# Optimization experiments

Measured on AMD Instinct MI355X. Metric: run time of the kernel, lower is better.

The kernel has to match this reference:

```python
import jax, jax.numpy as jnp
import numpy as np

B, N, C = 2, 384, 1024          # images, proposals/image, box_head feature dim
H_REPN = 256                    # RePN hidden
G_HID, HEADS = 256, 4           # GATConv hidden / heads
TOPK = 8
IMG_H, IMG_W = 800, 800
NEG_SLOPE = 0.2                 # PyG GATConv leaky_relu default


def _box_geom(bx):
    # normalized [x, y, w, h], matching _box_geom
    scale = jnp.array([IMG_W, IMG_H, IMG_W, IMG_H], dtype=bx.dtype)
    nb = bx / scale
    return jnp.stack([nb[:, 0], nb[:, 1], nb[:, 2] - nb[:, 0], nb[:, 3] - nb[:, 1]], axis=1)


def _gat_layer(x, src, tgt, W, att_src, att_dst, bias, heads, out_c):
    # PyG GATConv: messages flow src -> tgt, softmax over incoming edges at tgt
    n = x.shape[0]
    xw = (x @ W).reshape(n, heads, out_c)               # [N, H, F]
    a_s = jnp.sum(xw * att_src, axis=-1)                # [N, H]
    a_d = jnp.sum(xw * att_dst, axis=-1)                # [N, H]
    e = jax.nn.leaky_relu(a_s[src] + a_d[tgt], NEG_SLOPE)  # [E, H]
    e_max = jax.ops.segment_max(e, tgt, num_segments=n)    # stable softmax per target
    alpha = jnp.exp(e - e_max[tgt])
    denom = jax.ops.segment_sum(alpha, tgt, num_segments=n)
    alpha = alpha / jnp.maximum(denom, 1e-16)[tgt]          # [E, H]
    out = jax.ops.segment_sum(xw[src] * alpha[..., None], tgt, num_segments=n)
    return out.reshape(n, heads * out_c) + bias


def setup_inputs() -> dict:
    key = jax.random.key(0)
    ks = jax.random.split(key, 16)
    feats = jax.random.normal(ks[0], (B, N, C), dtype=jnp.float32)
    # boxes with x1<x2, y1<y2 inside the image
    xy = jax.random.uniform(ks[1], (B, N, 2), minval=0.0, maxval=650.0)
    wh = jax.random.uniform(ks[2], (B, N, 2), minval=10.0, maxval=150.0)
    boxes = jnp.concatenate([xy, xy + wh], axis=-1).astype(jnp.float32)
    s = 0.02
    params = {
        'fc1_w': jax.random.normal(ks[3], (2 * C + 4, H_REPN)) * s,
        'fc1_b': jnp.zeros((H_REPN,), jnp.float32),
        'fc2_w': jax.random.normal(ks[4], (H_REPN, 1)) * s,
        'fc2_b': jnp.zeros((1,), jnp.float32),
        'gat1_w': jax.random.normal(ks[5], (C + 4, HEADS * G_HID)) * s,
        'gat1_att_src': jax.random.normal(ks[6], (HEADS, G_HID)) * s,
        'gat1_att_dst': jax.random.normal(ks[7], (HEADS, G_HID)) * s,
        'gat1_b': jnp.zeros((HEADS * G_HID,), jnp.float32),
        'gat2_w': jax.random.normal(ks[8], (HEADS * G_HID, 2)) * s,
        'gat2_att_src': jax.random.normal(ks[9], (1, 2)) * s,
        'gat2_att_dst': jax.random.normal(ks[10], (1, 2)) * s,
        'gat2_b': jnp.zeros((2,), jnp.float32),
    }
    return {'feats': feats, 'boxes': boxes, **params}


def reference(feats, boxes, fc1_w, fc1_b, fc2_w, fc2_b,
              gat1_w, gat1_att_src, gat1_att_dst, gat1_b,
              gat2_w, gat2_att_src, gat2_att_dst, gat2_b):
    def single(f, bx):
        geom4 = _box_geom(bx)                               # [N, 4]
        x = jnp.concatenate([f, geom4], axis=1)             # [N, C+4]
        # RelationProposalNetwork: fc1(cat[f_i, f_j, |b_i-b_j|]) done as split matmuls
        Wa, Wb, Wg = fc1_w[:C], fc1_w[C:2 * C], fc1_w[2 * C:]
        p1 = f @ Wa                                         # [N, H]
        p2 = f @ Wb                                         # [N, H]
        gdiff = jnp.abs(bx[:, None, :] - bx[None, :, :])    # [N, N, 4]
        h = jax.nn.relu(p1[:, None, :] + p2[None, :, :] + gdiff @ Wg + fc1_b)
        rel = (h @ fc2_w)[..., 0] + fc2_b[0]                # [N, N]
        # _make_edge_index: mask diagonal, top-k per row; edge = [dst_node, neighbor]
        rn = rel - jnp.eye(N, dtype=rel.dtype) * 1e6
        nbr = jax.lax.top_k(rn, TOPK)[1]                    # [N, k]
        src = jnp.repeat(jnp.arange(N), TOPK)               # edge_index[0] (PyG source)
        tgt = nbr.reshape(-1)                               # edge_index[1] (PyG target)
        loop = jnp.arange(N)                                # GATConv add_self_loops=True
        src = jnp.concatenate([src, loop])
        tgt = jnp.concatenate([tgt, loop])
        h1 = jax.nn.relu(_gat_layer(x, src, tgt, gat1_w, gat1_att_src, gat1_att_dst, gat1_b, HEADS, G_HID))
        logits = _gat_layer(h1, src, tgt, gat2_w, gat2_att_src, gat2_att_dst, gat2_b, 1, 2)
        return logits                                       # [N, 2]
    return jax.vmap(single)(feats, boxes)
```

## Files before the change

### kernel.cpp

```cpp
#include <hip/hip_runtime.h>

#define BB 2
#define NN 384
#define CC 1024
#define HR 256
#define NHEADS 4
#define TOPK 8
#define CAP 448
#define NEG 0.2f

typedef __attribute__((ext_vector_type(8))) short bf16x8;
typedef __attribute__((ext_vector_type(4))) float f32x4;

__device__ __forceinline__ unsigned short f2bf(float v) {
    unsigned u = __float_as_uint(v);
    return (unsigned short)((u + 0x7FFFu + ((u >> 16) & 1u)) >> 16);
}
__device__ __forceinline__ float bf2f(unsigned short h) {
    return __uint_as_float((unsigned)h << 16);
}

__global__ __launch_bounds__(256) void k_prep(const float* __restrict__ feats,
        const float* __restrict__ boxes, const float* __restrict__ gat1_w,
        const float* __restrict__ fc1_w,
        uint4* __restrict__ Asw, uint4* __restrict__ Bsw,
        uint4* __restrict__ Ah, uint4* __restrict__ Al,
        uint4* __restrict__ Bh, uint4* __restrict__ Bl,
        float4* __restrict__ wgp, int* __restrict__ counts,
        float* __restrict__ xw2) {
    int blk = blockIdx.x;
    int t = threadIdx.x;
    int gflat = blk * 256 + t;
    if (gflat < BB * NN) counts[gflat] = 0;
    if (gflat < BB * NN * 2) xw2[gflat] = 0.f;

    if (blk < 396) {
        int flat = gflat;
        int lane = flat & 63;
        int kc = (flat >> 6) % 33;
        int mt = flat / (33 * 64);
        int m = mt * 16 + (lane & 15);
        int k0 = kc * 32 + (lane >> 4) * 8;
        unsigned short vals[8];
        const float s = 1.0f / 800.0f;
#pragma unroll
        for (int j = 0; j < 8; j++) {
            int k = k0 + j;
            float v;
            if (k < CC) v = feats[(size_t)m * CC + k];
            else if (k < CC + 4) {
                const float* bx = boxes + (size_t)m * 4;
                int gk = k - CC;
                v = (gk == 0) ? bx[0] * s : (gk == 1) ? bx[1] * s
                  : (gk == 2) ? (bx[2] - bx[0]) * s : (bx[3] - bx[1]) * s;
            } else v = 0.f;
            vals[j] = f2bf(v);
        }
        uint4 pk;
        pk.x = (unsigned)vals[0] | ((unsigned)vals[1] << 16);
        pk.y = (unsigned)vals[2] | ((unsigned)vals[3] << 16);
        pk.z = (unsigned)vals[4] | ((unsigned)vals[5] << 16);
        pk.w = (unsigned)vals[6] | ((unsigned)vals[7] << 16);
        Asw[flat] = pk;
    } else if (blk < 924) {
        int flat = gflat - 396 * 256;
        int lane = flat & 63;
        int kc = (flat >> 6) % 33;
        int nt = flat / (33 * 64);
        int n = nt * 16 + (lane & 15);
        int k0 = kc * 32 + (lane >> 4) * 8;
        unsigned short vals[8];
#pragma unroll
        for (int j = 0; j < 8; j++) {
            int k = k0 + j;
            float v = (k < CC + 4) ? gat1_w[(size_t)k * 1024 + n] : 0.f;
            vals[j] = f2bf(v);
        }
        uint4 pk;
        pk.x = (unsigned)vals[0] | ((unsigned)vals[1] << 16);
        pk.y = (unsigned)vals[2] | ((unsigned)vals[3] << 16);
        pk.z = (unsigned)vals[4] | ((unsigned)vals[5] << 16);
        pk.w = (unsigned)vals[6] | ((unsigned)vals[7] << 16);
        Bsw[flat] = pk;
    } else if (blk < 1308) {
        int flat = gflat - 924 * 256;
        int lane = flat & 63;
        int kc = (flat >> 6) % 32;
        int mt = flat / (32 * 64);
        int m = mt * 16 + (lane & 15);
        int k0 = kc * 32 + (lane >> 4) * 8;
        unsigned short vh[8], vl[8];
        const float* src = feats + (size_t)m * CC + k0;
#pragma unroll
        for (int j = 0; j < 8; j++) {
            float v = src[j];
            unsigned short h = f2bf(v);
            vh[j] = h;
            vl[j] = f2bf(v - bf2f(h));
        }
        uint4 ph, pl;
        ph.x = (unsigned)vh[0] | ((unsigned)vh[1] << 16);
        ph.y = (unsigned)vh[2] | ((unsigned)vh[3] << 16);
        ph.z = (unsigned)vh[4] | ((unsigned)vh[5] << 16);
        ph.w = (unsigned)vh[6] | ((unsigned)vh[7] << 16);
        pl.x = (unsigned)vl[0] | ((unsigned)vl[1] << 16);
        pl.y = (unsigned)vl[2] | ((unsigned)vl[3] << 16);
        pl.z = (unsigned)vl[4] | ((unsigned)vl[5] << 16);
        pl.w = (unsigned)vl[6] | ((unsigned)vl[7] << 16);
        Ah[flat] = ph; Al[flat] = pl;
    } else if (blk < 1564) {
        int flat = gflat - 1308 * 256;
        int lane = flat & 63;
        int kc = (flat >> 6) % 32;
        int nt = flat / (32 * 64);
        int n = nt * 16 + (lane & 15);
        int k0 = kc * 32 + (lane >> 4) * 8;
        unsigned short vh[8], vl[8];
#pragma unroll
        for (int j = 0; j < 8; j++) {
            int k = k0 + j;
            float v = (n < 256) ? fc1_w[(size_t)k * 256 + n]
                                : fc1_w[(size_t)(CC + k) * 256 + (n - 256)];
            unsigned short h = f2bf(v);
            vh[j] = h;
            vl[j] = f2bf(v - bf2f(h));
        }
        uint4 ph, pl;
        ph.x = (unsigned)vh[0] | ((unsigned)vh[1] << 16);
        ph.y = (unsigned)vh[2] | ((unsigned)vh[3] << 16);
        ph.z = (unsigned)vh[4] | ((unsigned)vh[5] << 16);
        ph.w = (unsigned)vh[6] | ((unsigned)vh[7] << 16);
        pl.x = (unsigned)vl[0] | ((unsigned)vl[1] << 16);
        pl.y = (unsigned)vl[2] | ((unsigned)vl[3] << 16);
        pl.z = (unsigned)vl[4] | ((unsigned)vl[5] << 16);
        pl.w = (unsigned)vl[6] | ((unsigned)vl[7] << 16);
        Bh[flat] = ph; Bl[flat] = pl;
    } else {
        int c = t;
        float4 w;
        w.x = fc1_w[(size_t)(2 * CC + 0) * HR + c];
        w.y = fc1_w[(size_t)(2 * CC + 1) * HR + c];
        w.z = fc1_w[(size_t)(2 * CC + 2) * HR + c];
        w.w = fc1_w[(size_t)(2 * CC + 3) * HR + c];
        wgp[c] = w;
    }
}

__global__ __launch_bounds__(512) void k_mm(const uint4* __restrict__ Ah,
        const uint4* __restrict__ Al, const uint4* __restrict__ Bh,
        const uint4* __restrict__ Bl, const float* __restrict__ fc1_b,
        float* __restrict__ p1, float* __restrict__ p2t,
        const uint4* __restrict__ Asw, const uint4* __restrict__ Bsw,
        float* __restrict__ xw1) {
    __shared__ float lds[4][64][4];
    int t = threadIdx.x;
    int w = t >> 6;
    int lane = t & 63;
    int g = w & 3;
    int kh = w >> 2;
    int blk0 = blockIdx.x;
    if (blk0 < 384) {
        int blk = blk0;
        int mt = blk >> 3;
        int nt = (blk & 7) * 4 + g;
        f32x4 acc = {0.f, 0.f, 0.f, 0.f};
        const uint4* pah = Ah + (size_t)mt * 32 * 64 + (size_t)kh * 16 * 64 + lane;
        const uint4* pal = Al + (size_t)mt * 32 * 64 + (size_t)kh * 16 * 64 + lane;
        const uint4* pbh = Bh + (size_t)nt * 32 * 64 + (size_t)kh * 16 * 64 + lane;
        const uint4* pbl = Bl + (size_t)nt * 32 * 64 + (size_t)kh * 16 * 64 + lane;
#pragma unroll 4
        for (int kc = 0; kc < 16; kc++) {
            uint4 ah = pah[kc * 64];
            uint4 al = pal[kc * 64];
            uint4 bh = pbh[kc * 64];
            uint4 bl = pbl[kc * 64];
            acc = __builtin_amdgcn_mfma_f32_16x16x32_bf16(*(bf16x8*)&ah, *(bf16x8*)&bh, acc, 0, 0, 0);
            acc = __builtin_amdgcn_mfma_f32_16x16x32_bf16(*(bf16x8*)&ah, *(bf16x8*)&bl, acc, 0, 0, 0);
            acc = __builtin_amdgcn_mfma_f32_16x16x32_bf16(*(bf16x8*)&al, *(bf16x8*)&bh, acc, 0, 0, 0);
        }
        if (kh == 1) {
#pragma unroll
            for (int r = 0; r < 4; r++) lds[g][lane][r] = acc[r];
        }
        __syncthreads();
        if (kh == 0) {
#pragma unroll
            for (int r = 0; r < 4; r++) acc[r] += lds[g][lane][r];
            int col = nt * 16 + (lane & 15);
            int row0 = mt * 16 + (lane >> 4) * 4;
            if (col < 256) {
                float bias = fc1_b[col];
#pragma unroll
                for (int r = 0; r < 4; r++)
                    p1[(size_t)(row0 + r) * 256 + col] = acc[r] + bias;
            } else {
#pragma unroll
                for (int r = 0; r < 4; r++) {
                    int rr = row0 + r;
                    int b = rr / NN, rloc = rr % NN;
                    p2t[((size_t)b * 256 + (col - 256)) * NN + rloc] = acc[r];
                }
            }
        }
    } else {
        int blk = blk0 - 384;
        int mt = blk >> 4;
        int nt = (blk & 15) * 4 + g;
        int nk = kh ? 16 : 17;
        f32x4 acc = {0.f, 0.f, 0.f, 0.f};
        const uint4* pa = Asw + (size_t)mt * 33 * 64 + (size_t)kh * 17 * 64 + lane;
        const uint4* pb = Bsw + (size_t)nt * 33 * 64 + (size_t)kh * 17 * 64 + lane;
#pragma unroll 4
        for (int kc = 0; kc < nk; kc++) {
            uint4 av = pa[kc * 64];
            uint4 bv = pb[kc * 64];
            acc = __builtin_amdgcn_mfma_f32_16x16x32_bf16(*(bf16x8*)&av, *(bf16x8*)&bv, acc, 0, 0, 0);
        }
        if (kh == 1) {
#pragma unroll
            for (int r = 0; r < 4; r++) lds[g][lane][r] = acc[r];
        }
        __syncthreads();
        if (kh == 0) {
#pragma unroll
            for (int r = 0; r < 4; r++) acc[r] += lds[g][lane][r];
            int col = nt * 16 + (lane & 15);
            int row0 = mt * 16 + (lane >> 4) * 4;
#pragma unroll
            for (int r = 0; r < 4; r++)
                xw1[(size_t)(row0 + r) * 1024 + col] = acc[r];
        }
    }
}

__global__ __launch_bounds__(384) void k_relatt(const float* __restrict__ p1,
        const float* __restrict__ p2t, const float* __restrict__ boxes,
        const float4* __restrict__ wgp, const float* __restrict__ fc2_w,
        float* __restrict__ rel_a, float* __restrict__ rel_b,
        const float* __restrict__ xw1, const float* __restrict__ att_src,
        const float* __restrict__ att_dst, float* __restrict__ a_s,
        float* __restrict__ a_d) {
    int blk0 = blockIdx.x;
    if (blk0 < 768) {
        int blk = blk0;
        int p = blk >> 1;
        int ch = blk & 1;
        int b = p / (NN / 2);
        int i0 = (p - b * (NN / 2)) * 2;
        int row0 = b * NN + i0;
        int j = threadIdx.x;
        float a0 = boxes[(size_t)row0 * 4 + 0];
        float a1 = boxes[(size_t)row0 * 4 + 1];
        float a2 = boxes[(size_t)row0 * 4 + 2];
        float a3 = boxes[(size_t)row0 * 4 + 3];
        float c0 = boxes[(size_t)(row0 + 1) * 4 + 0];
        float c1 = boxes[(size_t)(row0 + 1) * 4 + 1];
        float c2 = boxes[(size_t)(row0 + 1) * 4 + 2];
        float c3 = boxes[(size_t)(row0 + 1) * 4 + 3];
        float4 bj = *(const float4*)(boxes + ((size_t)b * NN + j) * 4);
        float g00 = fabsf(a0 - bj.x), g01 = fabsf(a1 - bj.y);
        float g02 = fabsf(a2 - bj.z), g03 = fabsf(a3 - bj.w);
        float g10 = fabsf(c0 - bj.x), g11 = fabsf(c1 - bj.y);
        float g12 = fabsf(c2 - bj.z), g13 = fabsf(c3 - bj.w);
        const float* p1r0 = p1 + (size_t)row0 * HR + ch * 128;
        const float* p1r1 = p1r0 + HR;
        const float* p2b = p2t + (size_t)b * HR * NN + (size_t)ch * 128 * NN + j;
        const float4* wg = wgp + ch * 128;
        const float* w2 = fc2_w + ch * 128;
        float acc0 = 0.f, acc1 = 0.f;
#pragma unroll 8
        for (int c = 0; c < 128; c++) {
            float4 w = wg[c];
            float pa = p1r0[c];
            float pb = p1r1[c];
            float wc = w2[c];
            float p2v = p2b[(size_t)c * NN];
            float v0 = pa + p2v + g00 * w.x + g01 * w.y + g02 * w.z + g03 * w.w;
            float v1 = pb + p2v + g10 * w.x + g11 * w.y + g12 * w.z + g13 * w.w;
            acc0 += fmaxf(v0, 0.f) * wc;
            acc1 += fmaxf(v1, 0.f) * wc;
        }
        float* dst = ch ? rel_b : rel_a;
        dst[(size_t)row0 * NN + j] = acc0;
        dst[(size_t)(row0 + 1) * NN + j] = acc1;
    } else {
        int node = blk0 - 768;
        int t = threadIdx.x;
        if (t >= 256) return;
        int w = t >> 6;
        int lane = t & 63;
        const float4* xr = (const float4*)(xw1 + (size_t)node * 1024 + w * 256);
        const float4* sr = (const float4*)(att_src + w * 256);
        const float4* dr = (const float4*)(att_dst + w * 256);
        float4 x = xr[lane];
        float4 s = sr[lane];
        float4 d = dr[lane];
        float ps = x.x * s.x + x.y * s.y + x.z * s.z + x.w * s.w;
        float pd = x.x * d.x + x.y * d.y + x.z * d.z + x.w * d.w;
#pragma unroll
        for (int off = 32; off > 0; off >>= 1) {
            ps += __shfl_xor(ps, off);
            pd += __shfl_xor(pd, off);
        }
        if (lane == 0) {
            a_s[(size_t)node * NHEADS + w] = ps;
            a_d[(size_t)node * NHEADS + w] = pd;
        }
    }
}

__global__ __launch_bounds__(64) void k_topk_inv(const float* __restrict__ rel_a,
        const float* __restrict__ rel_b, int* __restrict__ counts,
        int* __restrict__ inlist) {
    int row = blockIdx.x;
    int b = row / NN;
    int i = row - b * NN;
    int t = threadIdx.x;
    const float* ra = rel_a + (size_t)row * NN;
    const float* rb = rel_b + (size_t)row * NN;
    float v[6]; int id[6];
#pragma unroll
    for (int q = 0; q < 6; q++) {
        int j = t + q * 64;
        float val = ra[j] + rb[j];
        if (j == i) val = -INFINITY;
        v[q] = val; id[q] = j;
    }
    int mine = -1;
    for (int k = 0; k < TOPK; k++) {
        float bv = -INFINITY; int bi = NN;
#pragma unroll
        for (int q = 0; q < 6; q++) {
            if (v[q] > bv || (v[q] == bv && id[q] < bi)) { bv = v[q]; bi = id[q]; }
        }
        for (int off = 32; off > 0; off >>= 1) {
            float ov = __shfl_down(bv, off);
            int   oi = __shfl_down(bi, off);
            if (ov > bv || (ov == bv && oi < bi)) { bv = ov; bi = oi; }
        }
        bi = __shfl(bi, 0);
        if (t == k) mine = bi;
#pragma unroll
        for (int q = 0; q < 6; q++) if (id[q] == bi) v[q] = -INFINITY;
    }
    if (t < TOPK) {
        int tg = b * NN + mine;
        int q = atomicAdd(&counts[tg], 1);
        inlist[(size_t)tg * CAP + q] = i;
    } else if (t == TOPK) {
        int q = atomicAdd(&counts[row], 1);
        inlist[(size_t)row * CAP + q] = i;
    }
}

__global__ __launch_bounds__(256) void k_agg1h(const int* __restrict__ counts,
        const int* __restrict__ inlist, const float* __restrict__ a_s,
        const float* __restrict__ a_d, const float* __restrict__ xw1,
        const float* __restrict__ gat1_b, const float* __restrict__ w2,
        float* __restrict__ xw2) {
    __shared__ int slist[CAP];
    __shared__ float walpha[CAP];
    __shared__ float redp[8];
    int blk = blockIdx.x;
    int node = blk >> 2;
    int h = blk & 3;
    int b = node / NN;
    int t = threadIdx.x;
    int wid = t >> 6;
    int lane = t & 63;
    int deg = counts[node];
    for (int e = t; e < deg; e += 256) slist[e] = inlist[(size_t)node * CAP + e];
    __syncthreads();
    if (t < 64) {
        float ad = a_d[(size_t)node * NHEADS + h];
        float vals[7];
        int cnt = 0;
        float vmax = -INFINITY;
        for (int e = t; e < deg; e += 64) {
            float x = a_s[(size_t)(b * NN + slist[e]) * NHEADS + h] + ad;
            x = x >= 0.f ? x : NEG * x;
            vals[cnt++] = x;
            vmax = fmaxf(vmax, x);
        }
#pragma unroll
        for (int off = 32; off > 0; off >>= 1)
            vmax = fmaxf(vmax, __shfl_xor(vmax, off));
        float sum = 0.f;
        for (int i = 0; i < cnt; i++) {
            vals[i] = expf(vals[i] - vmax);
            sum += vals[i];
        }
#pragma unroll
        for (int off = 32; off > 0; off >>= 1)
            sum += __shfl_xor(sum, off);
        float inv = 1.f / fmaxf(sum, 1e-16f);
        cnt = 0;
        for (int e = t; e < deg; e += 64) walpha[e] = vals[cnt++] * inv;
    }
    __syncthreads();
    float acc = 0.f;
    for (int e = 0; e < deg; e++)
        acc += walpha[e] * xw1[(size_t)(b * NN + slist[e]) * 1024 + h * 256 + t];
    float o = fmaxf(acc + gat1_b[h * 256 + t], 0.f);
    int d = h * 256 + t;
    float p0 = o * w2[d * 2];
    float p1v = o * w2[d * 2 + 1];
#pragma unroll
    for (int off = 32; off > 0; off >>= 1) {
        p0 += __shfl_xor(p0, off);
        p1v += __shfl_xor(p1v, off);
    }
    if (lane == 0) { redp[wid] = p0; redp[4 + wid] = p1v; }
    __syncthreads();
    if (t == 0) {
        atomicAdd(&xw2[(size_t)node * 2],     redp[0] + redp[1] + redp[2] + redp[3]);
        atomicAdd(&xw2[(size_t)node * 2 + 1], redp[4] + redp[5] + redp[6] + redp[7]);
    }
}

__global__ __launch_bounds__(64) void k_agg2(const int* __restrict__ counts,
        const int* __restrict__ inlist, const float* __restrict__ xw2,
        const float* __restrict__ as2, const float* __restrict__ ad2,
        const float* __restrict__ b2, float* __restrict__ out) {
    int node = blockIdx.x;
    int b = node / NN;
    int lane = threadIdx.x;
    int deg = counts[node];
    float s0 = as2[0], s1 = as2[1];
    float d0 = ad2[0], d1 = ad2[1];
    float2 xwn = *(const float2*)(xw2 + (size_t)node * 2);
    float ad = xwn.x * d0 + xwn.y * d1;
    float vals[7], xs0[7], xs1[7];
    int cnt = 0;
    float vmax = -INFINITY;
    for (int e = lane; e < deg; e += 64) {
        int s = b * NN + inlist[(size_t)node * CAP + e];
        float2 xws = *(const float2*)(xw2 + (size_t)s * 2);
        float x = xws.x * s0 + xws.y * s1 + ad;
        x = x >= 0.f ? x : NEG * x;
        xs0[cnt] = xws.x; xs1[cnt] = xws.y; vals[cnt] = x; cnt++;
        vmax = fmaxf(vmax, x);
    }
#pragma unroll
    for (int off = 32; off > 0; off >>= 1)
        vmax = fmaxf(vmax, __shfl_xor(vmax, off));
    float sum = 0.f;
    for (int i = 0; i < cnt; i++) {
        vals[i] = expf(vals[i] - vmax);
        sum += vals[i];
    }
#pragma unroll
    for (int off = 32; off > 0; off >>= 1)
        sum += __shfl_xor(sum, off);
    float inv = 1.f / fmaxf(sum, 1e-16f);
    float a0 = 0.f, a1 = 0.f;
    for (int i = 0; i < cnt; i++) {
        a0 += vals[i] * xs0[i];
        a1 += vals[i] * xs1[i];
    }
#pragma unroll
    for (int off = 32; off > 0; off >>= 1) {
        a0 += __shfl_xor(a0, off);
        a1 += __shfl_xor(a1, off);
    }
    if (lane == 0) {
        out[(size_t)node * 2]     = a0 * inv + b2[0];
        out[(size_t)node * 2 + 1] = a1 * inv + b2[1];
    }
}

extern "C" void kernel_launch(void* const* d_in, const int* in_sizes, int n_in,
                              void* d_out, int out_size, void* d_ws, size_t ws_size,
                              hipStream_t stream) {
    const float* feats  = (const float*)d_in[0];
    const float* boxes  = (const float*)d_in[1];
    const float* fc1_w  = (const float*)d_in[2];
    const float* fc1_b  = (const float*)d_in[3];
    const float* fc2_w  = (const float*)d_in[4];
    const float* fc2_b  = (const float*)d_in[5];
    const float* gat1_w = (const float*)d_in[6];
    const float* g1as   = (const float*)d_in[7];
    const float* g1ad   = (const float*)d_in[8];
    const float* gat1_b = (const float*)d_in[9];
    const float* gat2_w = (const float*)d_in[10];
    const float* g2as   = (const float*)d_in[11];
    const float* g2ad   = (const float*)d_in[12];
    const float* gat2_b = (const float*)d_in[13];
    float* out = (float*)d_out;
    (void)fc2_b;

    char* ws = (char*)d_ws;
    size_t off = 0;
    auto alloc = [&](size_t bytes) -> void* {
        void* p = ws + off;
        off += (bytes + 255) / 256 * 256;
        return p;
    };
    int*   counts = (int*)alloc((size_t)BB * NN * 4);
    int*   inlist = (int*)alloc((size_t)BB * NN * CAP * 4);
    float* p1     = (float*)alloc((size_t)BB * NN * HR * 4);
    float* p2t    = (float*)alloc((size_t)BB * HR * NN * 4);
    float* rel_a  = (float*)alloc((size_t)BB * NN * NN * 4);
    float* rel_b  = (float*)alloc((size_t)BB * NN * NN * 4);
    float* xw1    = (float*)alloc((size_t)BB * NN * 1024 * 4);
    float* a_s1   = (float*)alloc((size_t)BB * NN * NHEADS * 4);
    float* a_d1   = (float*)alloc((size_t)BB * NN * NHEADS * 4);
    float* xw2    = (float*)alloc((size_t)BB * NN * 2 * 4);
    uint4* Asw    = (uint4*)alloc((size_t)48 * 33 * 64 * 16);
    uint4* Bsw    = (uint4*)alloc((size_t)64 * 33 * 64 * 16);
    uint4* Ah     = (uint4*)alloc((size_t)48 * 32 * 64 * 16);
    uint4* Al     = (uint4*)alloc((size_t)48 * 32 * 64 * 16);
    uint4* Bh     = (uint4*)alloc((size_t)32 * 32 * 64 * 16);
    uint4* Bl     = (uint4*)alloc((size_t)32 * 32 * 64 * 16);
    float4* wgp   = (float4*)alloc((size_t)HR * 16);
    (void)ws_size; (void)in_sizes; (void)n_in; (void)out_size;

    k_prep<<<1565, 256, 0, stream>>>(feats, boxes, gat1_w, fc1_w,
                                     Asw, Bsw, Ah, Al, Bh, Bl, wgp, counts, xw2);
    k_mm<<<1152, 512, 0, stream>>>(Ah, Al, Bh, Bl, fc1_b, p1, p2t, Asw, Bsw, xw1);
    k_relatt<<<1536, 384, 0, stream>>>(p1, p2t, boxes, wgp, fc2_w, rel_a, rel_b,
                                       xw1, g1as, g1ad, a_s1, a_d1);
    k_topk_inv<<<BB * NN, 64, 0, stream>>>(rel_a, rel_b, counts, inlist);
    k_agg1h<<<BB * NN * NHEADS, 256, 0, stream>>>(counts, inlist, a_s1, a_d1, xw1,
                                                  gat1_b, gat2_w, xw2);
    k_agg2<<<BB * NN, 64, 0, stream>>>(counts, inlist, xw2, g2as, g2ad, gat2_b, out);
}
```

Baseline: 162.4 us.

## Coalesce weight swizzle via LDS transpose and compute two M-tiles per wave

The weight-prep branches now stage a 32x64 tile of gat1_w/fc1_w in shared memory with row-coalesced reads, then emit the MFMA-swizzled bf16 layout from LDS. Before, each lane read strided columns. The matmul kernel makes each wave compute two adjacent 16-row M tiles that share the B fragment, which halves B loads per output and halves the grid to 576 blocks. The costs are more registers and fewer blocks available to hide latency.

```diff
diff --git a/kernel.cpp b/kernel.cpp
--- a/kernel.cpp
+++ b/kernel.cpp
@@ -28,6 +28,7 @@
         uint4* __restrict__ Bh, uint4* __restrict__ Bl,
         float4* __restrict__ wgp, int* __restrict__ counts,
         float* __restrict__ xw2) {
+    __shared__ float sw[32][65];
     int blk = blockIdx.x;
     int t = threadIdx.x;
     int gflat = blk * 256 + t;
@@ -63,25 +64,35 @@
         pk.w = (unsigned)vals[6] | ((unsigned)vals[7] << 16);
         Asw[flat] = pk;
     } else if (blk < 924) {
-        int flat = gflat - 396 * 256;
-        int lane = flat & 63;
-        int kc = (flat >> 6) % 33;
-        int nt = flat / (33 * 64);
-        int n = nt * 16 + (lane & 15);
-        int k0 = kc * 32 + (lane >> 4) * 8;
+        int blkrel = blk - 396;
+        int ntg = blkrel / 33;
+        int kc  = blkrel % 33;
+        int k0 = kc * 32;
+        int n0 = ntg * 64;
+#pragma unroll
+        for (int pass = 0; pass < 8; pass++) {
+            int kl = pass * 4 + (t >> 6);
+            int k = k0 + kl;
+            int nl = t & 63;
+            float v = (k < CC + 4) ? gat1_w[(size_t)k * 1024 + n0 + nl] : 0.f;
+            sw[kl][nl] = v;
+        }
+        __syncthreads();
+        int local_nt = t >> 6;
+        int lane = t & 63;
+        int nn = lane & 15;
+        int q = lane >> 4;
+        int nl = local_nt * 16 + nn;
         unsigned short vals[8];
 #pragma unroll
-        for (int j = 0; j < 8; j++) {
-            int k = k0 + j;
-            float v = (k < CC + 4) ? gat1_w[(size_t)k * 1024 + n] : 0.f;
-            vals[j] = f2bf(v);
-        }
+        for (int j = 0; j < 8; j++) vals[j] = f2bf(sw[q * 8 + j][nl]);
         uint4 pk;
         pk.x = (unsigned)vals[0] | ((unsigned)vals[1] << 16);
         pk.y = (unsigned)vals[2] | ((unsigned)vals[3] << 16);
         pk.z = (unsigned)vals[4] | ((unsigned)vals[5] << 16);
         pk.w = (unsigned)vals[6] | ((unsigned)vals[7] << 16);
-        Bsw[flat] = pk;
+        int nt = ntg * 4 + local_nt;
+        Bsw[(size_t)nt * 33 * 64 + kc * 64 + lane] = pk;
     } else if (blk < 1308) {
         int flat = gflat - 924 * 256;
         int lane = flat & 63;
@@ -109,18 +120,30 @@
         pl.w = (unsigned)vl[6] | ((unsigned)vl[7] << 16);
         Ah[flat] = ph; Al[flat] = pl;
     } else if (blk < 1564) {
-        int flat = gflat - 1308 * 256;
-        int lane = flat & 63;
-        int kc = (flat >> 6) % 32;
-        int nt = flat / (32 * 64);
-        int n = nt * 16 + (lane & 15);
-        int k0 = kc * 32 + (lane >> 4) * 8;
-        unsigned short vh[8], vl[8];
-#pragma unroll
-        for (int j = 0; j < 8; j++) {
-            int k = k0 + j;
+        int blkrel = blk - 1308;
+        int ntg = blkrel / 32;
+        int kc  = blkrel % 32;
+        int k0 = kc * 32;
+        int n0 = ntg * 64;
+#pragma unroll
+        for (int pass = 0; pass < 8; pass++) {
+            int kl = pass * 4 + (t >> 6);
+            int k = k0 + kl;
+            int n = n0 + (t & 63);
             float v = (n < 256) ? fc1_w[(size_t)k * 256 + n]
                                 : fc1_w[(size_t)(CC + k) * 256 + (n - 256)];
+            sw[kl][t & 63] = v;
+        }
+        __syncthreads();
+        int local_nt = t >> 6;
+        int lane = t & 63;
+        int nn = lane & 15;
+        int q = lane >> 4;
+        int nl = local_nt * 16 + nn;
+        unsigned short vh[8], vl[8];
+#pragma unroll
+        for (int j = 0; j < 8; j++) {
+            float v = sw[q * 8 + j][nl];
             unsigned short h = f2bf(v);
             vh[j] = h;
             vl[j] = f2bf(v - bf2f(h));
@@ -134,7 +157,9 @@
         pl.y = (unsigned)vl[2] | ((unsigned)vl[3] << 16);
         pl.z = (unsigned)vl[4] | ((unsigned)vl[5] << 16);
         pl.w = (unsigned)vl[6] | ((unsigned)vl[7] << 16);
-        Bh[flat] = ph; Bl[flat] = pl;
+        int nt = ntg * 4 + local_nt;
+        size_t o = (size_t)nt * 32 * 64 + kc * 64 + lane;
+        Bh[o] = ph; Bl[o] = pl;
     } else {
         int c = t;
         float4 w;
@@ -152,83 +177,98 @@
         float* __restrict__ p1, float* __restrict__ p2t,
         const uint4* __restrict__ Asw, const uint4* __restrict__ Bsw,
         float* __restrict__ xw1) {
-    __shared__ float lds[4][64][4];
+    __shared__ float lds[4][64][8];
     int t = threadIdx.x;
     int w = t >> 6;
     int lane = t & 63;
     int g = w & 3;
     int kh = w >> 2;
     int blk0 = blockIdx.x;
-    if (blk0 < 384) {
-        int blk = blk0;
-        int mt = blk >> 3;
-        int nt = (blk & 7) * 4 + g;
-        f32x4 acc = {0.f, 0.f, 0.f, 0.f};
-        const uint4* pah = Ah + (size_t)mt * 32 * 64 + (size_t)kh * 16 * 64 + lane;
-        const uint4* pal = Al + (size_t)mt * 32 * 64 + (size_t)kh * 16 * 64 + lane;
+    if (blk0 < 192) {
+        int mtp = blk0 >> 3;
+        int nt = (blk0 & 7) * 4 + g;
+        int mt0 = mtp * 2;
+        f32x4 acc0 = {0.f, 0.f, 0.f, 0.f};
+        f32x4 acc1 = {0.f, 0.f, 0.f, 0.f};
+        const uint4* pah0 = Ah + (size_t)mt0 * 32 * 64 + (size_t)kh * 16 * 64 + lane;
+        const uint4* pal0 = Al + (size_t)mt0 * 32 * 64 + (size_t)kh * 16 * 64 + lane;
         const uint4* pbh = Bh + (size_t)nt * 32 * 64 + (size_t)kh * 16 * 64 + lane;
         const uint4* pbl = Bl + (size_t)nt * 32 * 64 + (size_t)kh * 16 * 64 + lane;
-#pragma unroll 4
+#pragma unroll 2
         for (int kc = 0; kc < 16; kc++) {
-            uint4 ah = pah[kc * 64];
-            uint4 al = pal[kc * 64];
+            uint4 ah0 = pah0[kc * 64];
+            uint4 al0 = pal0[kc * 64];
+            uint4 ah1 = pah0[kc * 64 + 2048];
+            uint4 al1 = pal0[kc * 64 + 2048];
             uint4 bh = pbh[kc * 64];
             uint4 bl = pbl[kc * 64];
-            acc = __builtin_amdgcn_mfma_f32_16x16x32_bf16(*(bf16x8*)&ah, *(bf16x8*)&bh, acc, 0, 0, 0);
-            acc = __builtin_amdgcn_mfma_f32_16x16x32_bf16(*(bf16x8*)&ah, *(bf16x8*)&bl, acc, 0, 0, 0);
-            acc = __builtin_amdgcn_mfma_f32_16x16x32_bf16(*(bf16x8*)&al, *(bf16x8*)&bh, acc, 0, 0, 0);
+            acc0 = __builtin_amdgcn_mfma_f32_16x16x32_bf16(*(bf16x8*)&ah0, *(bf16x8*)&bh, acc0, 0, 0, 0);
+            acc0 = __builtin_amdgcn_mfma_f32_16x16x32_bf16(*(bf16x8*)&ah0, *(bf16x8*)&bl, acc0, 0, 0, 0);
+            acc0 = __builtin_amdgcn_mfma_f32_16x16x32_bf16(*(bf16x8*)&al0, *(bf16x8*)&bh, acc0, 0, 0, 0);
+            acc1 = __builtin_amdgcn_mfma_f32_16x16x32_bf16(*(bf16x8*)&ah1, *(bf16x8*)&bh, acc1, 0, 0, 0);
+            acc1 = __builtin_amdgcn_mfma_f32_16x16x32_bf16(*(bf16x8*)&ah1, *(bf16x8*)&bl, acc1, 0, 0, 0);
+            acc1 = __builtin_amdgcn_mfma_f32_16x16x32_bf16(*(bf16x8*)&al1, *(bf16x8*)&bh, acc1, 0, 0, 0);
         }
         if (kh == 1) {
 #pragma unroll
-            for (int r = 0; r < 4; r++) lds[g][lane][r] = acc[r];
+            for (int r = 0; r < 4; r++) { lds[g][lane][r] = acc0[r]; lds[g][lane][4 + r] = acc1[r]; }
         }
         __syncthreads();
         if (kh == 0) {
 #pragma unroll
-            for (int r = 0; r < 4; r++) acc[r] += lds[g][lane][r];
+            for (int r = 0; r < 4; r++) { acc0[r] += lds[g][lane][r]; acc1[r] += lds[g][lane][4 + r]; }
             int col = nt * 16 + (lane & 15);
-            int row0 = mt * 16 + (lane >> 4) * 4;
+            int rbase = (lane >> 4) * 4;
             if (col < 256) {
                 float bias = fc1_b[col];
 #pragma unroll
-                for (int r = 0; r < 4; r++)
-                    p1[(size_t)(row0 + r) * 256 + col] = acc[r] + bias;
+                for (int r = 0; r < 4; r++) {
+                    p1[(size_t)(mt0 * 16 + rbase + r) * 256 + col] = acc0[r] + bias;
+                    p1[(size_t)(mt0 * 16 + 16 + rbase + r) * 256 + col] = acc1[r] + bias;
+                }
             } else {
 #pragma unroll
                 for (int r = 0; r < 4; r++) {
-                    int rr = row0 + r;
-                    int b = rr / NN, rloc = rr % NN;
-                    p2t[((size_t)b * 256 + (col - 256)) * NN + rloc] = acc[r];
+                    int rr0 = mt0 * 16 + rbase + r;
+                    int rr1 = rr0 + 16;
+                    p2t[((size_t)(rr0 / NN) * 256 + (col - 256)) * NN + (rr0 % NN)] = acc0[r];
+                    p2t[((size_t)(rr1 / NN) * 256 + (col - 256)) * NN + (rr1 % NN)] = acc1[r];
                 }
             }
         }
     } else {
-        int blk = blk0 - 384;
-        int mt = blk >> 4;
+        int blk = blk0 - 192;
+        int mtp = blk >> 4;
         int nt = (blk & 15) * 4 + g;
+        int mt0 = mtp * 2;
         int nk = kh ? 16 : 17;
-        f32x4 acc = {0.f, 0.f, 0.f, 0.f};
-        const uint4* pa = Asw + (size_t)mt * 33 * 64 + (size_t)kh * 17 * 64 + lane;
+        f32x4 acc0 = {0.f, 0.f, 0.f, 0.f};
+        f32x4 acc1 = {0.f, 0.f, 0.f, 0.f};
+        const uint4* pa0 = Asw + (size_t)mt0 * 33 * 64 + (size_t)kh * 17 * 64 + lane;
         const uint4* pb = Bsw + (size_t)nt * 33 * 64 + (size_t)kh * 17 * 64 + lane;
 #pragma unroll 4
         for (int kc = 0; kc < nk; kc++) {
-            uint4 av = pa[kc * 64];
+            uint4 a0 = pa0[kc * 64];
+            uint4 a1 = pa0[kc * 64 + 2112];
             uint4 bv = pb[kc * 64];
-            acc = __builtin_amdgcn_mfma_f32_16x16x32_bf16(*(bf16x8*)&av, *(bf16x8*)&bv, acc, 0, 0, 0);
+            acc0 = __builtin_amdgcn_mfma_f32_16x16x32_bf16(*(bf16x8*)&a0, *(bf16x8*)&bv, acc0, 0, 0, 0);
+            acc1 = __builtin_amdgcn_mfma_f32_16x16x32_bf16(*(bf16x8*)&a1, *(bf16x8*)&bv, acc1, 0, 0, 0);
         }
         if (kh == 1) {
 #pragma unroll
-            for (int r = 0; r < 4; r++) lds[g][lane][r] = acc[r];
+            for (int r = 0; r < 4; r++) { lds[g][lane][r] = acc0[r]; lds[g][lane][4 + r] = acc1[r]; }
         }
         __syncthreads();
         if (kh == 0) {
 #pragma unroll
-            for (int r = 0; r < 4; r++) acc[r] += lds[g][lane][r];
+            for (int r = 0; r < 4; r++) { acc0[r] += lds[g][lane][r]; acc1[r] += lds[g][lane][4 + r]; }
             int col = nt * 16 + (lane & 15);
-            int row0 = mt * 16 + (lane >> 4) * 4;
-#pragma unroll
-            for (int r = 0; r < 4; r++)
-                xw1[(size_t)(row0 + r) * 1024 + col] = acc[r];
+            int rbase = (lane >> 4) * 4;
+#pragma unroll
+            for (int r = 0; r < 4; r++) {
+                xw1[(size_t)(mt0 * 16 + rbase + r) * 1024 + col] = acc0[r];
+                xw1[(size_t)(mt0 * 16 + 16 + rbase + r) * 1024 + col] = acc1[r];
+            }
         }
     }
 }
@@ -517,7 +557,7 @@
 
     k_prep<<<1565, 256, 0, stream>>>(feats, boxes, gat1_w, fc1_w,
                                      Asw, Bsw, Ah, Al, Bh, Bl, wgp, counts, xw2);
-    k_mm<<<1152, 512, 0, stream>>>(Ah, Al, Bh, Bl, fc1_b, p1, p2t, Asw, Bsw, xw1);
+    k_mm<<<576, 512, 0, stream>>>(Ah, Al, Bh, Bl, fc1_b, p1, p2t, Asw, Bsw, xw1);
     k_relatt<<<1536, 384, 0, stream>>>(p1, p2t, boxes, wgp, fc2_w, rel_a, rel_b,
                                        xw1, g1as, g1ad, a_s1, a_d1);
     k_topk_inv<<<BB * NN, 64, 0, stream>>>(rel_a, rel_b, counts, inlist);
```

New measurement: 160.9 us, median of 2. Within noise of the previous version (-0.9%).
